# Performance work log

Measured on AMD Instinct MI355X. Metric: run time of the kernel, lower is better.

Reference implementation:

```python
import jax, jax.numpy as jnp
import numpy as np

B, P, ENC, DEC, ATT, EMB, V, MAXLEN = 64, 196, 2048, 1024, 1024, 1024, 10000, 20


def setup_inputs() -> dict:
    key = jax.random.key(0)
    ks = jax.random.split(key, 20)
    s = 0.02
    inp = {
        'encoder_out': jax.random.normal(ks[0], (B, 14, 14, ENC), jnp.float32),
        'encoded_captions': jax.random.randint(ks[1], (B, MAXLEN), 0, V),
        'caption_lengths': jax.random.randint(ks[2], (B, 1), 2, MAXLEN + 1).at[0, 0].set(MAXLEN),
        # embedding
        'emb_table': jax.random.uniform(ks[3], (V, EMB), jnp.float32, -0.1, 0.1),
        # attention MLP (weight_norm Linear == plain Linear math)
        'We': jax.random.normal(ks[4], (ATT, ENC)) * s,
        'be': jnp.zeros((ATT,), jnp.float32),
        'Wd': jax.random.normal(ks[5], (ATT, DEC)) * s,
        'bd': jnp.zeros((ATT,), jnp.float32),
        'Wf': jax.random.normal(ks[6], (1, ATT)) * s,
        'bf': jnp.zeros((1,), jnp.float32),
        # top_down_attention LSTMCell: input = EMB+ENC+DEC
        'W_ih1': jax.random.normal(ks[7], (4 * DEC, EMB + ENC + DEC)) * s,
        'W_hh1': jax.random.normal(ks[8], (4 * DEC, DEC)) * s,
        'b_ih1': jnp.zeros((4 * DEC,), jnp.float32),
        'b_hh1': jnp.zeros((4 * DEC,), jnp.float32),
        # language_model LSTMCell: input = ENC+DEC
        'W_ih2': jax.random.normal(ks[9], (4 * DEC, ENC + DEC)) * s,
        'W_hh2': jax.random.normal(ks[10], (4 * DEC, DEC)) * s,
        'b_ih2': jnp.zeros((4 * DEC,), jnp.float32),
        'b_hh2': jnp.zeros((4 * DEC,), jnp.float32),
        # output heads
        'Wfc1': jax.random.normal(ks[11], (V, DEC)) * s,
        'bfc1': jnp.zeros((V,), jnp.float32),
        'Wfc': jax.random.uniform(ks[12], (V, DEC), jnp.float32, -0.1, 0.1),
        'bfc': jnp.zeros((V,), jnp.float32),
    }
    return inp


def _lstm_cell(x, h, c, Wih, Whh, bih, bhh):
    g = x @ Wih.T + bih + h @ Whh.T + bhh
    i, f, gg, o = jnp.split(g, 4, axis=-1)  # torch gate order: i, f, g, o
    c2 = jax.nn.sigmoid(f) * c + jax.nn.sigmoid(i) * jnp.tanh(gg)
    h2 = jax.nn.sigmoid(o) * jnp.tanh(c2)
    return h2, c2


def _decode(encoder_out, encoded_captions, caption_lengths, emb_table,
            We, be, Wd, bd, Wf, bf,
            W_ih1, W_hh1, b_ih1, b_hh1, W_ih2, W_hh2, b_ih2, b_hh2,
            Wfc1, bfc1, Wfc, bfc):
    b = encoder_out.shape[0]
    enc = encoder_out.reshape(b, -1, encoder_out.shape[-1])  # (B,P,ENC)
    enc_mean = enc.mean(axis=1)
    cl = caption_lengths.squeeze(1)
    sort_ind = jnp.argsort(-cl)
    cl = cl[sort_ind]
    enc = enc[sort_ind]
    enc_mean = enc_mean[sort_ind]
    caps = encoded_captions[sort_ind]
    dec_len = cl - 1  # (B,)
    embeds = emb_table[caps]  # (B,T,EMB)
    Tdec = caps.shape[1] - 1
    # precompute encoder attention projection (loop-invariant, same math)
    att1 = jnp.einsum('bpe,ae->bpa', enc, We) + be  # (B,P,ATT)

    def step(carry, t):
        h1, c1, h2, c2 = carry
        active = (t < dec_len)[:, None]  # (B,1)
        x1 = jnp.concatenate([h2, enc_mean, embeds[:, t, :]], axis=1)
        h1n, c1n = _lstm_cell(x1, h1, c1, W_ih1, W_hh1, b_ih1, b_hh1)
        h1n = jnp.where(active, h1n, h1)
        c1n = jnp.where(active, c1n, c1)
        # Bahdanau attention
        att2 = h1n @ Wd.T + bd  # (B,ATT)
        e = jnp.einsum('bpa,a->bp', jax.nn.relu(att1 + att2[:, None, :]), Wf[0]) + bf[0]
        alpha = jax.nn.softmax(e, axis=1)
        awe = jnp.einsum('bpe,bp->be', enc, alpha)
        preds1 = h1n @ Wfc1.T + bfc1  # dropout is identity at eval
        x2 = jnp.concatenate([awe, h1n], axis=1)
        h2n, c2n = _lstm_cell(x2, h2, c2, W_ih2, W_hh2, b_ih2, b_hh2)
        h2n = jnp.where(active, h2n, h2)
        c2n = jnp.where(active, c2n, c2)
        preds = h2n @ Wfc.T + bfc
        preds = jnp.where(active, preds, 0.0)
        preds1 = jnp.where(active, preds1, 0.0)
        return (h1n, c1n, h2n, c2n), (preds, preds1)

    z = jnp.zeros((b, DEC), jnp.float32)
    (_, _, _, _), (pr, pr1) = jax.lax.scan(step, (z, z, z, z), jnp.arange(Tdec))
    predictions = jnp.transpose(pr, (1, 0, 2))  # (B,Tdec,V)
    predictions1 = jnp.transpose(pr1, (1, 0, 2))
    return predictions, predictions1, caps, dec_len, sort_ind


def reference(encoder_out, encoded_captions, caption_lengths, emb_table,
              We, be, Wd, bd, Wf, bf,
              W_ih1, W_hh1, b_ih1, b_hh1, W_ih2, W_hh2, b_ih2, b_hh2,
              Wfc1, bfc1, Wfc, bfc):
    return _decode(encoder_out, encoded_captions, caption_lengths, emb_table,
                   We, be, Wd, bd, Wf, bf,
                   W_ih1, W_hh1, b_ih1, b_hh1, W_ih2, W_hh2, b_ih2, b_hh2,
                   Wfc1, bfc1, Wfc, bfc)
```

## Files before the change

### kernel.cpp

```cpp
#include <hip/hip_runtime.h>
#include <cmath>

#define B_ 64
#define P_ 196
#define ENC_ 2048
#define DEC_ 1024
#define V_ 10000
#define MAXLEN_ 20
#define TDEC_ 19

typedef __attribute__((ext_vector_type(8))) short bf16x8;
typedef __attribute__((ext_vector_type(4))) float f32x4;


__device__ __align__(16) short g_encb[(size_t)12544 * 2048];
__device__ __align__(16) short g_encbt[(size_t)12544 * 2048];
__device__ __align__(16) short g_att1[(size_t)12544 * 1024];
__device__ __align__(16) short g_Wp1t[(size_t)4096 * 2048];
__device__ __align__(16) short g_Wemt[(size_t)4096 * 2048];
__device__ __align__(16) short g_Wembt[(size_t)4096 * 1024];
__device__ __align__(16) short g_Wc2t[(size_t)4096 * 4096];
__device__ __align__(16) short g_Webt[(size_t)1024 * 2048];
__device__ __align__(16) short g_Wdt[(size_t)1024 * 1024];
__device__ __align__(16) short g_Wfc1t[(size_t)10000 * 1024];
__device__ __align__(16) short g_Wfct[(size_t)10000 * 1024];
__device__ __align__(16) short g_xs1[(size_t)20 * 64 * 2048];
__device__ __align__(16) short g_xemb[(size_t)19 * 64 * 1024];
__device__ __align__(16) short g_xc2[(size_t)20 * 64 * 4096];
__device__ __align__(16) short g_em[64 * 2048];
__device__ __align__(16) float g_preemb[(size_t)19 * 64 * 4096];
__device__ __align__(16) float g_preem[64 * 4096];
__device__ __align__(16) float g_part[(size_t)16 * 64 * 4096];
__device__ __align__(16) float g_att2p[(size_t)8 * 64 * 1024];
__device__ __align__(16) float g_e[64 * P_];
__device__ __align__(16) float g_c1[64 * 1024];
__device__ __align__(16) float g_c2[64 * 1024];
__device__ int g_ibuf[64 + 64 + 64 * MAXLEN_];

__device__ __forceinline__ short f2b(float f) {
  unsigned u = __float_as_uint(f);
  u += 0x7FFFu + ((u >> 16) & 1u);
  return (short)(u >> 16);
}
__device__ __forceinline__ float b2f(short s) {
  return __uint_as_float(((unsigned)(unsigned short)s) << 16);
}

__global__ void k_sort(const int* __restrict__ cl_in, const int* __restrict__ caps_in,
                       int* __restrict__ sind, int* __restrict__ declen, int* __restrict__ caps_s,
                       float* __restrict__ out_caps, float* __restrict__ out_declen,
                       float* __restrict__ out_sind) {
  int i = threadIdx.x;
  __shared__ int cl[B_];
  cl[i] = cl_in[i];
  __syncthreads();
  int my = cl[i], pos = 0;
  for (int j = 0; j < B_; ++j) {
    int cj = cl[j];
    if (cj > my || (cj == my && j < i)) pos++;
  }
  sind[pos] = i;
  __syncthreads();
  int sb = sind[i];
  int dl = cl[sb] - 1;
  declen[i] = dl;
  out_declen[i] = (float)dl;
  out_sind[i] = (float)sb;
  for (int t = 0; t < MAXLEN_; ++t) {
    int v = caps_in[sb * MAXLEN_ + t];
    caps_s[i * MAXLEN_ + t] = v;
    out_caps[i * MAXLEN_ + t] = (float)v;
  }
}

__global__ __launch_bounds__(256) void k_encprep(const float* __restrict__ enc,
                                                 const int* __restrict__ sind,
                                                 short* __restrict__ encb,
                                                 short* __restrict__ encbt) {
  int mg = blockIdx.x;
  int b = mg / P_, p = mg - b * P_;
  int tid = threadIdx.x;
  const float* src = enc + ((size_t)sind[b] * P_ + p) * ENC_ + tid * 8;
  float4 a = *(const float4*)src;
  float4 c = *(const float4*)(src + 4);
  bf16x8 v;
  v[0] = f2b(a.x); v[1] = f2b(a.y); v[2] = f2b(a.z); v[3] = f2b(a.w);
  v[4] = f2b(c.x); v[5] = f2b(c.y); v[6] = f2b(c.z); v[7] = f2b(c.w);
  *(bf16x8*)(encb + (size_t)mg * ENC_ + tid * 8) = v;
  size_t off = (((size_t)(mg >> 4) * 64 + (tid >> 2)) << 9) +
               (((mg & 15) | ((tid & 3) << 4)) << 3);
  *(bf16x8*)(encbt + off) = v;
}

__global__ __launch_bounds__(64) void k_encmeanb(const short* __restrict__ encb,
                                                 short* __restrict__ em) {
  int b = blockIdx.x;
  int col0 = blockIdx.y * 512 + threadIdx.x * 8;
  const short* src = encb + (size_t)b * P_ * ENC_ + col0;
  float acc[8] = {};
  for (int p = 0; p < P_; ++p) {
    bf16x8 v = *(const bf16x8*)(src + (size_t)p * ENC_);
#pragma unroll
    for (int j = 0; j < 8; ++j) acc[j] += b2f(v[j]);
  }
#pragma unroll
  for (int j = 0; j < 8; ++j) em[b * 2048 + col0 + j] = f2b(acc[j] * (1.0f / 196.0f));
}

__global__ __launch_bounds__(256) void k_prefill(const float* __restrict__ emb,
                                                 const int* __restrict__ caps_s,
                                                 short* __restrict__ xemb) {
  int t = blockIdx.x, b = blockIdx.y, tid = threadIdx.x;
  short* xr = xemb + ((size_t)t * 64 + b) * 1024;
  int cap = caps_s[b * MAXLEN_ + t];
  int j = tid * 4;
  float4 v = *(const float4*)(emb + (size_t)cap * 1024 + j);
  short4 o;
  o.x = f2b(v.x); o.y = f2b(v.y); o.z = f2b(v.z); o.w = f2b(v.w);
  *(short4*)(xr + j) = o;
}

struct F2BJobs {
  const float* src[10];
  short* dst[10];
  int kstride[10];
  int c0[10];
  int ncols[10];
  int ktot[10];
  int koff[10];
  int base[11];
};

__global__ __launch_bounds__(256) void k_f2bt_all(F2BJobs jb) {
  int bg = blockIdx.x;
  int j = 0;
#pragma unroll
  for (int q = 1; q < 10; ++q)
    if (bg >= jb.base[q]) j = q;
  int wave = threadIdx.x >> 6, lane = threadIdx.x & 63;
  int tau = (bg - jb.base[j]) * 4 + wave;
  int ntk = jb.ncols[j] >> 5;
  int rt = tau / ntk, kt = tau - rt * ntk;
  int r = rt * 16 + (lane & 15);
  int k8 = kt * 32 + (lane >> 4) * 8;
  const float* s = jb.src[j] + (size_t)r * jb.kstride[j] + jb.c0[j] + k8;
  float4 a = *(const float4*)s;
  float4 c = *(const float4*)(s + 4);
  bf16x8 v;
  v[0] = f2b(a.x); v[1] = f2b(a.y); v[2] = f2b(a.z); v[3] = f2b(a.w);
  v[4] = f2b(c.x); v[5] = f2b(c.y); v[6] = f2b(c.z); v[7] = f2b(c.w);
  int kg0 = jb.koff[j] + kt * 32;
  size_t toff = (((size_t)rt * (jb.ktot[j] >> 5) + (kg0 >> 5)) << 9);
  *(bf16x8*)(jb.dst[j] + toff + lane * 8) = v;
}

__global__ __launch_bounds__(512) void k_att1_t(const short* __restrict__ At,
                                                const short* __restrict__ Wt,
                                                const float* __restrict__ be,
                                                short* __restrict__ Cb) {
  int wave = threadIdx.x >> 6, lane = threadIdx.x & 63;
  int mt0 = blockIdx.x * 8 + (wave >> 2) * 4;
  int nt0 = blockIdx.y * 16 + (wave & 3) * 4;
  f32x4 acc[4][4] = {};
  const short* Ab = At + ((size_t)mt0 * 64 << 9) + lane * 8;
  const short* Wb = Wt + ((size_t)nt0 * 64 << 9) + lane * 8;
  for (int kt = 0; kt < 64; ++kt) {
    bf16x8 a[4], b[4];
#pragma unroll
    for (int i = 0; i < 4; ++i) a[i] = *(const bf16x8*)(Ab + (((size_t)i * 64 + kt) << 9));
#pragma unroll
    for (int j = 0; j < 4; ++j) b[j] = *(const bf16x8*)(Wb + (((size_t)j * 64 + kt) << 9));
#pragma unroll
    for (int i = 0; i < 4; ++i)
#pragma unroll
      for (int j = 0; j < 4; ++j)
        acc[i][j] = __builtin_amdgcn_mfma_f32_16x16x32_bf16(a[i], b[j], acc[i][j], 0, 0, 0);
  }
  int rr = (lane >> 4) * 4, cc = lane & 15;
  int m0 = mt0 * 16, n0 = nt0 * 16;
#pragma unroll
  for (int i = 0; i < 4; ++i)
#pragma unroll
    for (int j = 0; j < 4; ++j) {
      int n = n0 + j * 16 + cc;
      float bn = be[n];
#pragma unroll
      for (int r = 0; r < 4; ++r) {
        int m = m0 + i * 16 + rr + r;
        Cb[(size_t)m * 1024 + n] = f2b(acc[i][j][r] + bn);
      }
    }
}

__global__ __launch_bounds__(256) void k_skinny_t(const short* __restrict__ A, int lda,
                                                  const short* __restrict__ Wt, int ldw,
                                                  int N, int kchunk, float* __restrict__ part) {
  int wave = threadIdx.x >> 6, lane = threadIdx.x & 63;
  int n0 = blockIdx.x * 128 + wave * 32;
  int kb = blockIdx.y * kchunk;
  int lr = lane & 15, lk = (lane >> 4) * 8;
  int ntk = ldw >> 5;
  int nt0 = n0 >> 4;
  f32x4 acc[4][2] = {};
  const short* Ab = A + (size_t)lr * lda + kb + lk;
  const short* Wb0 = Wt + (((size_t)nt0 * ntk + (kb >> 5)) << 9) + lane * 8;
  const short* Wb1 = Wt + (((size_t)(nt0 + 1) * ntk + (kb >> 5)) << 9) + lane * 8;
  int nkt = kchunk >> 5;
  for (int kt = 0; kt < nkt; ++kt) {
    bf16x8 a[4], b0, b1;
#pragma unroll
    for (int i = 0; i < 4; ++i) a[i] = *(const bf16x8*)(Ab + (size_t)i * 16 * lda + kt * 32);
    b0 = *(const bf16x8*)(Wb0 + ((size_t)kt << 9));
    b1 = *(const bf16x8*)(Wb1 + ((size_t)kt << 9));
#pragma unroll
    for (int i = 0; i < 4; ++i) {
      acc[i][0] = __builtin_amdgcn_mfma_f32_16x16x32_bf16(a[i], b0, acc[i][0], 0, 0, 0);
      acc[i][1] = __builtin_amdgcn_mfma_f32_16x16x32_bf16(a[i], b1, acc[i][1], 0, 0, 0);
    }
  }
  float* po = part + (size_t)blockIdx.y * 64 * N;
  int rr = (lane >> 4) * 4, cc = lane & 15;
#pragma unroll
  for (int i = 0; i < 4; ++i)
#pragma unroll
    for (int j = 0; j < 2; ++j) {
      int n = n0 + j * 16 + cc;
#pragma unroll
      for (int r = 0; r < 4; ++r) {
        int m = i * 16 + rr + r;
        po[(size_t)m * N + n] = acc[i][j][r];
      }
    }
}

__global__ void k_sumn(const float* __restrict__ part, int nsplit, float* __restrict__ dst) {
  int idx = blockIdx.x * 256 + threadIdx.x;
  float s = 0.0f;
  for (int q = 0; q < nsplit; ++q) s += part[(size_t)q * 64 * 4096 + idx];
  dst[idx] = s;
}

__global__ __launch_bounds__(256) void k_mid_emb4(const short* __restrict__ xemb,
                                                  const short* __restrict__ Wt,
                                                  float* __restrict__ preemb) {
  int wg = blockIdx.x;
  wg = (wg & 7) * 38 + (wg >> 3);
  int t = wg % 19;
  int nch = wg / 19;
  const short* A = xemb + (size_t)t * 64 * 1024;
  int wave = threadIdx.x >> 6, lane = threadIdx.x & 63;
  int nt0 = nch * 16 + wave * 4;
  int lr = lane & 15, lk = (lane >> 4) * 8;
  f32x4 acc[4][4] = {};
  const short* Ab = A + (size_t)lr * 1024 + lk;
  const short* Wb[4];
#pragma unroll
  for (int j = 0; j < 4; ++j) Wb[j] = Wt + ((size_t)(nt0 + j) * 32 << 9) + lane * 8;
  for (int kt = 0; kt < 32; ++kt) {
    bf16x8 a[4], b[4];
#pragma unroll
    for (int j = 0; j < 4; ++j) b[j] = *(const bf16x8*)(Wb[j] + ((size_t)kt << 9));
#pragma unroll
    for (int i = 0; i < 4; ++i) a[i] = *(const bf16x8*)(Ab + (size_t)i * 16 * 1024 + kt * 32);
#pragma unroll
    for (int i = 0; i < 4; ++i)
#pragma unroll
      for (int j = 0; j < 4; ++j)
        acc[i][j] = __builtin_amdgcn_mfma_f32_16x16x32_bf16(a[i], b[j], acc[i][j], 0, 0, 0);
  }
  float* po = preemb + (size_t)t * 64 * 4096;
  int rr = (lane >> 4) * 4, cc = lane & 15;
#pragma unroll
  for (int i = 0; i < 4; ++i)
#pragma unroll
    for (int j = 0; j < 4; ++j) {
      int n = (nt0 + j) * 16 + cc;
#pragma unroll
      for (int r = 0; r < 4; ++r) {
        int m = i * 16 + rr + r;
        po[(size_t)m * 4096 + n] = acc[i][j][r];
      }
    }
}

__global__ void k_gates(const float* __restrict__ part, int nsplit,
                        const float* __restrict__ pre, const float* __restrict__ pre2,
                        const float* __restrict__ bih, const float* __restrict__ bhh,
                        float* __restrict__ c,
                        const short* __restrict__ hold, int ldo,
                        short* __restrict__ dst1, int ld1,
                        short* __restrict__ dst2, int ld2,
                        const int* __restrict__ declen, int t) {
  int idx = blockIdx.x * 256 + threadIdx.x;
  int b = idx >> 10, j = idx & 1023;
  const float* pb = part + (size_t)b * 4096;
  float gi = bih[j] + bhh[j];
  float gf = bih[1024 + j] + bhh[1024 + j];
  float gg = bih[2048 + j] + bhh[2048 + j];
  float go = bih[3072 + j] + bhh[3072 + j];
  if (pre) {
    const float* pp = pre + (size_t)b * 4096;
    gi += pp[j]; gf += pp[j + 1024]; gg += pp[j + 2048]; go += pp[j + 3072];
  }
  if (pre2) {
    const float* pp = pre2 + (size_t)b * 4096;
    gi += pp[j]; gf += pp[j + 1024]; gg += pp[j + 2048]; go += pp[j + 3072];
  }
  for (int s = 0; s < nsplit; ++s) {
    const float* p = pb + (size_t)s * 64 * 4096;
    gi += p[j]; gf += p[j + 1024]; gg += p[j + 2048]; go += p[j + 3072];
  }
  float si = 1.0f / (1.0f + expf(-gi));
  float sf = 1.0f / (1.0f + expf(-gf));
  float so = 1.0f / (1.0f + expf(-go));
  float cn = sf * c[idx] + si * tanhf(gg);
  float hn = so * tanhf(cn);
  short hb;
  if (t < declen[b]) {
    c[idx] = cn;
    hb = f2b(hn);
  } else {
    hb = hold[b * ldo + j];
  }
  dst1[b * ld1 + j] = hb;
  dst2[b * ld2 + j] = hb;
}

__global__ __launch_bounds__(256) void k_e(const short* __restrict__ att1,
                                           const float* __restrict__ att2p,
                                           const float* __restrict__ bd,
                                           const float* __restrict__ Wf,
                                           const float* __restrict__ bf,
                                           float* __restrict__ e) {
  __shared__ float a2[1024];
  int b = blockIdx.x / 13, pq = blockIdx.x % 13;
  for (int i = threadIdx.x; i < 1024; i += 256) {
    float s = bd[i];
#pragma unroll
    for (int q = 0; q < 4; ++q) s += att2p[q * 65536 + b * 1024 + i];
    a2[i] = s;
  }
  __syncthreads();
  int wave = threadIdx.x >> 6, lane = threadIdx.x & 63;
#pragma unroll
  for (int i = 0; i < 4; ++i) {
    int p = pq * 16 + wave * 4 + i;
    if (p >= P_) break;
    const short* a1 = att1 + ((size_t)(b * P_ + p)) * 1024;
    float s = 0.0f;
#pragma unroll
    for (int h = 0; h < 2; ++h) {
      int k0 = lane * 8 + h * 512;
      bf16x8 v = *(const bf16x8*)(a1 + k0);
#pragma unroll
      for (int j = 0; j < 8; ++j) s += Wf[k0 + j] * fmaxf(b2f(v[j]) + a2[k0 + j], 0.0f);
    }
#pragma unroll
    for (int off = 32; off; off >>= 1) s += __shfl_down(s, off);
    if (lane == 0) e[b * P_ + p] = s + bf[0];
  }
}

__global__ __launch_bounds__(256) void k_sawe(const float* __restrict__ e,
                                              const short* __restrict__ encb,
                                              short* __restrict__ xc2t) {
  int b = blockIdx.x, ch = blockIdx.y;
  __shared__ float al[P_];
  __shared__ float red[8][256];
  int tid = threadIdx.x;
  if (tid < 64) {
    float vals[4];
    float mx = -1e30f;
#pragma unroll
    for (int q = 0; q < 4; ++q) {
      int p = tid + q * 64;
      vals[q] = (p < P_) ? e[b * P_ + p] : -1e30f;
      mx = fmaxf(mx, vals[q]);
    }
#pragma unroll
    for (int off = 32; off; off >>= 1) mx = fmaxf(mx, __shfl_xor(mx, off));
    float sum = 0.0f;
#pragma unroll
    for (int q = 0; q < 4; ++q) {
      int p = tid + q * 64;
      vals[q] = (p < P_) ? expf(vals[q] - mx) : 0.0f;
      sum += vals[q];
    }
#pragma unroll
    for (int off = 32; off; off >>= 1) sum += __shfl_xor(sum, off);
    float inv = 1.0f / sum;
#pragma unroll
    for (int q = 0; q < 4; ++q) {
      int p = tid + q * 64;
      if (p < P_) al[p] = vals[q] * inv;
    }
  }
  __syncthreads();
  int pg = tid >> 5, cg = tid & 31;
  int col = ch * 256 + cg * 8;
  const short* src = encb + (size_t)b * P_ * ENC_ + col;
  float acc[8] = {};
  for (int p = pg; p < P_; p += 8) {
    bf16x8 v = *(const bf16x8*)(src + (size_t)p * ENC_);
    float ap = al[p];
#pragma unroll
    for (int j = 0; j < 8; ++j) acc[j] += ap * b2f(v[j]);
  }
#pragma unroll
  for (int j = 0; j < 8; ++j) red[pg][cg * 8 + j] = acc[j];
  __syncthreads();
  float s = 0.0f;
#pragma unroll
  for (int g = 0; g < 8; ++g) s += red[g][tid];
  xc2t[b * 4096 + ch * 256 + tid] = f2b(s);
}

__global__ __launch_bounds__(256) void k_head4(const short* __restrict__ Aall,
                                               const short* __restrict__ Wt,
                                               const float* __restrict__ bias,
                                               float* __restrict__ outp,
                                               const int* __restrict__ declen) {
  int wg = blockIdx.x;
  wg = (wg & 7) * 95 + (wg >> 3);
  int t = wg % 19;
  int nch = wg / 19;
  const short* A = Aall + (size_t)t * (64 * 4096);
  int wave = threadIdx.x >> 6, lane = threadIdx.x & 63;
  int nt0 = nch * 16 + wave * 4;
  int lr = lane & 15, lk = (lane >> 4) * 8;
  f32x4 acc[4][4] = {};
  const short* Ab = A + (size_t)lr * 4096 + lk;
  const short* Wb[4];
  bool ok[4];
#pragma unroll
  for (int j = 0; j < 4; ++j) {
    ok[j] = (nt0 + j) < (V_ >> 4);
    Wb[j] = Wt + ((size_t)(ok[j] ? nt0 + j : 0) * 32 << 9) + lane * 8;
  }
  for (int kt = 0; kt < 32; ++kt) {
    bf16x8 a[4], b[4];
#pragma unroll
    for (int j = 0; j < 4; ++j) b[j] = *(const bf16x8*)(Wb[j] + ((size_t)kt << 9));
#pragma unroll
    for (int i = 0; i < 4; ++i) a[i] = *(const bf16x8*)(Ab + (size_t)i * 16 * 4096 + kt * 32);
#pragma unroll
    for (int i = 0; i < 4; ++i)
#pragma unroll
      for (int j = 0; j < 4; ++j)
        acc[i][j] = __builtin_amdgcn_mfma_f32_16x16x32_bf16(a[i], b[j], acc[i][j], 0, 0, 0);
  }
  int rr = (lane >> 4) * 4, cc = lane & 15;
#pragma unroll
  for (int j = 0; j < 4; ++j) {
    if (!ok[j]) continue;
    int n = (nt0 + j) * 16 + cc;
    float bn = bias[n];
#pragma unroll
    for (int i = 0; i < 4; ++i) {
#pragma unroll
      for (int r = 0; r < 4; ++r) {
        int b = i * 16 + rr + r;
        float val = acc[i][j][r] + bn;
        outp[((size_t)b * TDEC_ + t) * V_ + n] = (t < declen[b]) ? val : 0.0f;
      }
    }
  }
}

extern "C" void kernel_launch(void* const* d_in, const int* in_sizes, int n_in,
                              void* d_out, int out_size, void* d_ws, size_t ws_size,
                              hipStream_t stream) {
  (void)in_sizes; (void)n_in; (void)d_ws; (void)ws_size; (void)out_size;
  const float* enc  = (const float*)d_in[0];
  const int*   caps = (const int*)d_in[1];
  const int*   cl   = (const int*)d_in[2];
  const float* emb  = (const float*)d_in[3];
  const float* We   = (const float*)d_in[4];
  const float* be   = (const float*)d_in[5];
  const float* Wd   = (const float*)d_in[6];
  const float* bd   = (const float*)d_in[7];
  const float* Wf   = (const float*)d_in[8];
  const float* bf   = (const float*)d_in[9];
  const float* Wih1 = (const float*)d_in[10];
  const float* Whh1 = (const float*)d_in[11];
  const float* bih1 = (const float*)d_in[12];
  const float* bhh1 = (const float*)d_in[13];
  const float* Wih2 = (const float*)d_in[14];
  const float* Whh2 = (const float*)d_in[15];
  const float* bih2 = (const float*)d_in[16];
  const float* bhh2 = (const float*)d_in[17];
  const float* Wfc1 = (const float*)d_in[18];
  const float* bfc1 = (const float*)d_in[19];
  const float* Wfc  = (const float*)d_in[20];
  const float* bfc  = (const float*)d_in[21];
  float* out = (float*)d_out;

  short *encb, *encbt, *att1, *Wp1t, *Wemt, *Wembt, *Wc2t, *Webt, *Wdt, *Wfc1t, *Wfct;
  short *xs1, *xemb, *xc2, *em;
  float *preemb, *preem, *part, *att2p, *e, *c1, *c2;
  int* ib;
  hipGetSymbolAddress((void**)&encb, HIP_SYMBOL(g_encb));
  hipGetSymbolAddress((void**)&encbt, HIP_SYMBOL(g_encbt));
  hipGetSymbolAddress((void**)&att1, HIP_SYMBOL(g_att1));
  hipGetSymbolAddress((void**)&Wp1t, HIP_SYMBOL(g_Wp1t));
  hipGetSymbolAddress((void**)&Wemt, HIP_SYMBOL(g_Wemt));
  hipGetSymbolAddress((void**)&Wembt, HIP_SYMBOL(g_Wembt));
  hipGetSymbolAddress((void**)&Wc2t, HIP_SYMBOL(g_Wc2t));
  hipGetSymbolAddress((void**)&Webt, HIP_SYMBOL(g_Webt));
  hipGetSymbolAddress((void**)&Wdt, HIP_SYMBOL(g_Wdt));
  hipGetSymbolAddress((void**)&Wfc1t, HIP_SYMBOL(g_Wfc1t));
  hipGetSymbolAddress((void**)&Wfct, HIP_SYMBOL(g_Wfct));
  hipGetSymbolAddress((void**)&xs1, HIP_SYMBOL(g_xs1));
  hipGetSymbolAddress((void**)&xemb, HIP_SYMBOL(g_xemb));
  hipGetSymbolAddress((void**)&xc2, HIP_SYMBOL(g_xc2));
  hipGetSymbolAddress((void**)&em, HIP_SYMBOL(g_em));
  hipGetSymbolAddress((void**)&preemb, HIP_SYMBOL(g_preemb));
  hipGetSymbolAddress((void**)&preem, HIP_SYMBOL(g_preem));
  hipGetSymbolAddress((void**)&part, HIP_SYMBOL(g_part));
  hipGetSymbolAddress((void**)&att2p, HIP_SYMBOL(g_att2p));
  hipGetSymbolAddress((void**)&e, HIP_SYMBOL(g_e));
  hipGetSymbolAddress((void**)&c1, HIP_SYMBOL(g_c1));
  hipGetSymbolAddress((void**)&c2, HIP_SYMBOL(g_c2));
  hipGetSymbolAddress((void**)&ib, HIP_SYMBOL(g_ibuf));
  int* sind = ib;
  int* declen = ib + 64;
  int* caps_s = ib + 128;

  float* out_preds  = out;
  float* out_preds1 = out + (size_t)B_ * TDEC_ * V_;
  float* out_caps   = out + 2ull * B_ * TDEC_ * V_;
  float* out_declen = out_caps + B_ * MAXLEN_;
  float* out_sind   = out_declen + B_;

  k_sort<<<1, 64, 0, stream>>>(cl, caps, sind, declen, caps_s, out_caps, out_declen, out_sind);
  hipMemsetAsync(c1, 0, 64 * 1024 * sizeof(float), stream);
  hipMemsetAsync(c2, 0, 64 * 1024 * sizeof(float), stream);
  hipMemsetAsync(xs1, 0, (size_t)64 * 2048 * sizeof(short), stream);
  hipMemsetAsync(xc2, 0, (size_t)64 * 4096 * sizeof(short), stream);
  k_encprep<<<12544, 256, 0, stream>>>(enc, sind, encb, encbt);
  k_encmeanb<<<dim3(64, 4), 64, 0, stream>>>(encb, em);
  k_prefill<<<dim3(19, 64), 256, 0, stream>>>(emb, caps_s, xemb);
  {
    F2BJobs jb;
    const float* srcs[10] = {Wih1, Whh1, Wih1, Wih1, Wih2, Whh2, We, Wd, Wfc1, Wfc};
    short* dsts[10] = {Wp1t, Wp1t, Wemt, Wembt, Wc2t, Wc2t, Webt, Wdt, Wfc1t, Wfct};
    int kstride[10] = {4096, 1024, 4096, 4096, 3072, 1024, 2048, 1024, 1024, 1024};
    int c0s[10]     = {0, 0, 1024, 3072, 0, 0, 0, 0, 0, 0};
    int ncols[10]   = {1024, 1024, 2048, 1024, 3072, 1024, 2048, 1024, 1024, 1024};
    int ktots[10]   = {2048, 2048, 2048, 1024, 4096, 4096, 2048, 1024, 1024, 1024};
    int koffs[10]   = {0, 1024, 0, 0, 0, 3072, 0, 0, 0, 0};
    int nblk[10]    = {2048, 2048, 4096, 2048, 6144, 2048, 1024, 512, 5000, 5000};
    int cum = 0;
    for (int q = 0; q < 10; ++q) {
      jb.src[q] = srcs[q]; jb.dst[q] = dsts[q];
      jb.kstride[q] = kstride[q]; jb.c0[q] = c0s[q]; jb.ncols[q] = ncols[q];
      jb.ktot[q] = ktots[q]; jb.koff[q] = koffs[q];
      jb.base[q] = cum; cum += nblk[q];
    }
    jb.base[10] = cum;
    k_f2bt_all<<<cum, 256, 0, stream>>>(jb);
  }
  k_att1_t<<<dim3(98, 4), 512, 0, stream>>>(encbt, Webt, be, att1);
  k_skinny_t<<<dim3(32, 4), 256, 0, stream>>>(em, 2048, Wemt, 2048, 4096, 512, part);
  k_sumn<<<1024, 256, 0, stream>>>(part, 4, preem);
  k_mid_emb4<<<304, 256, 0, stream>>>(xemb, Wembt, preemb);

  for (int t = 0; t < TDEC_; ++t) {
    short* s1t = xs1 + (size_t)t * 64 * 2048;
    short* s1n = xs1 + (size_t)(t + 1) * 64 * 2048;
    short* x2t = xc2 + (size_t)t * 64 * 4096;
    short* x2n = xc2 + (size_t)(t + 1) * 64 * 4096;
    k_skinny_t<<<dim3(32, 8), 256, 0, stream>>>(s1t, 2048, Wp1t, 2048, 4096, 256, part);
    k_gates<<<256, 256, 0, stream>>>(part, 8, preemb + (size_t)t * 64 * 4096, preem,
                                     bih1, bhh1, c1, s1t + 1024, 2048,
                                     s1n + 1024, 2048, x2t + 2048, 4096, declen, t);
    k_skinny_t<<<dim3(8, 4), 256, 0, stream>>>(x2t + 2048, 4096, Wdt, 1024, 1024, 256, att2p);
    k_e<<<832, 256, 0, stream>>>(att1, att2p, bd, Wf, bf, e);
    k_sawe<<<dim3(64, 8), 256, 0, stream>>>(e, encb, x2t);
    k_skinny_t<<<dim3(32, 8), 256, 0, stream>>>(x2t, 4096, Wc2t, 4096, 4096, 512, part);
    k_gates<<<256, 256, 0, stream>>>(part, 8, nullptr, nullptr, bih2, bhh2, c2, s1t, 2048,
                                     s1n, 2048, x2n + 3072, 4096, declen, t);
  }
  k_head4<<<760, 256, 0, stream>>>(xc2 + 2048, Wfc1t, bfc1, out_preds1, declen);
  k_head4<<<760, 256, 0, stream>>>(xc2 + 64 * 4096 + 3072, Wfct, bfc, out_preds, declen);
}
```

Baseline: 1.696 ms.

## Fuse per-timestep decoder loop into one persistent cooperative kernel with grid syncs

Replaces the 19×7 separate kernel launches of the recurrent decode loop with a single cooperative kernel of 256 blocks that runs every phase (skinny GEMMs, gates, attention energy, softmax-weighted sum) and separates them with grid.sync(). This removes launch overhead and inter-kernel gaps on the serial critical path. In exchange, phases that used more blocks (k_e with 832, k_sawe with 512) now loop over work items inside fewer blocks. Small phases leave most blocks idle while they wait at the grid barrier.

```diff
diff --git a/kernel.cpp b/kernel.cpp
--- a/kernel.cpp
+++ b/kernel.cpp
@@ -1,5 +1,8 @@
 #include <hip/hip_runtime.h>
+#include <hip/hip_cooperative_groups.h>
 #include <cmath>
+
+namespace cg = cooperative_groups;
 
 #define B_ 64
 #define P_ 196
@@ -192,12 +195,12 @@
     }
 }
 
-__global__ __launch_bounds__(256) void k_skinny_t(const short* __restrict__ A, int lda,
-                                                  const short* __restrict__ Wt, int ldw,
-                                                  int N, int kchunk, float* __restrict__ part) {
-  int wave = threadIdx.x >> 6, lane = threadIdx.x & 63;
-  int n0 = blockIdx.x * 128 + wave * 32;
-  int kb = blockIdx.y * kchunk;
+__device__ __forceinline__ void skinny_phase(const short* __restrict__ A, int lda,
+                                             const short* __restrict__ Wt, int ldw,
+                                             int N, int kchunk, float* __restrict__ part,
+                                             int bx, int by, int wave, int lane) {
+  int n0 = bx * 128 + wave * 32;
+  int kb = by * kchunk;
   int lr = lane & 15, lk = (lane >> 4) * 8;
   int ntk = ldw >> 5;
   int nt0 = n0 >> 4;
@@ -218,7 +221,7 @@
       acc[i][1] = __builtin_amdgcn_mfma_f32_16x16x32_bf16(a[i], b1, acc[i][1], 0, 0, 0);
     }
   }
-  float* po = part + (size_t)blockIdx.y * 64 * N;
+  float* po = part + (size_t)by * 64 * N;
   int rr = (lane >> 4) * 4, cc = lane & 15;
 #pragma unroll
   for (int i = 0; i < 4; ++i)
@@ -231,6 +234,13 @@
         po[(size_t)m * N + n] = acc[i][j][r];
       }
     }
+}
+
+__global__ __launch_bounds__(256) void k_skinny_t(const short* __restrict__ A, int lda,
+                                                  const short* __restrict__ Wt, int ldw,
+                                                  int N, int kchunk, float* __restrict__ part) {
+  skinny_phase(A, lda, Wt, ldw, N, kchunk, part, blockIdx.x, blockIdx.y,
+               threadIdx.x >> 6, threadIdx.x & 63);
 }
 
 __global__ void k_sumn(const float* __restrict__ part, int nsplit, float* __restrict__ dst) {
@@ -283,15 +293,15 @@
     }
 }
 
-__global__ void k_gates(const float* __restrict__ part, int nsplit,
+__device__ __forceinline__ void gates_phase(const float* __restrict__ part, int nsplit,
                         const float* __restrict__ pre, const float* __restrict__ pre2,
                         const float* __restrict__ bih, const float* __restrict__ bhh,
                         float* __restrict__ c,
                         const short* __restrict__ hold, int ldo,
                         short* __restrict__ dst1, int ld1,
                         short* __restrict__ dst2, int ld2,
-                        const int* __restrict__ declen, int t) {
-  int idx = blockIdx.x * 256 + threadIdx.x;
+                        const int* __restrict__ declen, int t, int bid, int tid) {
+  int idx = bid * 256 + tid;
   int b = idx >> 10, j = idx & 1023;
   const float* pb = part + (size_t)b * 4096;
   float gi = bih[j] + bhh[j];
@@ -326,93 +336,123 @@
   dst2[b * ld2 + j] = hb;
 }
 
-__global__ __launch_bounds__(256) void k_e(const short* __restrict__ att1,
-                                           const float* __restrict__ att2p,
-                                           const float* __restrict__ bd,
-                                           const float* __restrict__ Wf,
-                                           const float* __restrict__ bf,
-                                           float* __restrict__ e) {
-  __shared__ float a2[1024];
-  int b = blockIdx.x / 13, pq = blockIdx.x % 13;
-  for (int i = threadIdx.x; i < 1024; i += 256) {
-    float s = bd[i];
-#pragma unroll
-    for (int q = 0; q < 4; ++q) s += att2p[q * 65536 + b * 1024 + i];
-    a2[i] = s;
-  }
-  __syncthreads();
-  int wave = threadIdx.x >> 6, lane = threadIdx.x & 63;
-#pragma unroll
-  for (int i = 0; i < 4; ++i) {
-    int p = pq * 16 + wave * 4 + i;
-    if (p >= P_) break;
-    const short* a1 = att1 + ((size_t)(b * P_ + p)) * 1024;
-    float s = 0.0f;
-#pragma unroll
-    for (int h = 0; h < 2; ++h) {
-      int k0 = lane * 8 + h * 512;
-      bf16x8 v = *(const bf16x8*)(a1 + k0);
-#pragma unroll
-      for (int j = 0; j < 8; ++j) s += Wf[k0 + j] * fmaxf(b2f(v[j]) + a2[k0 + j], 0.0f);
-    }
-#pragma unroll
-    for (int off = 32; off; off >>= 1) s += __shfl_down(s, off);
-    if (lane == 0) e[b * P_ + p] = s + bf[0];
-  }
-}
-
-__global__ __launch_bounds__(256) void k_sawe(const float* __restrict__ e,
-                                              const short* __restrict__ encb,
-                                              short* __restrict__ xc2t) {
-  int b = blockIdx.x, ch = blockIdx.y;
-  __shared__ float al[P_];
-  __shared__ float red[8][256];
-  int tid = threadIdx.x;
-  if (tid < 64) {
-    float vals[4];
-    float mx = -1e30f;
-#pragma unroll
-    for (int q = 0; q < 4; ++q) {
-      int p = tid + q * 64;
-      vals[q] = (p < P_) ? e[b * P_ + p] : -1e30f;
-      mx = fmaxf(mx, vals[q]);
-    }
-#pragma unroll
-    for (int off = 32; off; off >>= 1) mx = fmaxf(mx, __shfl_xor(mx, off));
-    float sum = 0.0f;
-#pragma unroll
-    for (int q = 0; q < 4; ++q) {
-      int p = tid + q * 64;
-      vals[q] = (p < P_) ? expf(vals[q] - mx) : 0.0f;
-      sum += vals[q];
-    }
-#pragma unroll
-    for (int off = 32; off; off >>= 1) sum += __shfl_xor(sum, off);
-    float inv = 1.0f / sum;
-#pragma unroll
-    for (int q = 0; q < 4; ++q) {
-      int p = tid + q * 64;
-      if (p < P_) al[p] = vals[q] * inv;
-    }
-  }
-  __syncthreads();
-  int pg = tid >> 5, cg = tid & 31;
-  int col = ch * 256 + cg * 8;
-  const short* src = encb + (size_t)b * P_ * ENC_ + col;
-  float acc[8] = {};
-  for (int p = pg; p < P_; p += 8) {
-    bf16x8 v = *(const bf16x8*)(src + (size_t)p * ENC_);
-    float ap = al[p];
-#pragma unroll
-    for (int j = 0; j < 8; ++j) acc[j] += ap * b2f(v[j]);
-  }
-#pragma unroll
-  for (int j = 0; j < 8; ++j) red[pg][cg * 8 + j] = acc[j];
-  __syncthreads();
-  float s = 0.0f;
-#pragma unroll
-  for (int g = 0; g < 8; ++g) s += red[g][tid];
-  xc2t[b * 4096 + ch * 256 + tid] = f2b(s);
+struct LoopArgs {
+  const short *Wp1t, *Wc2t, *Wdt, *att1, *encb;
+  const float *preemb, *preem, *bih1, *bhh1, *bih2, *bhh2, *bd, *Wf, *bf;
+  short *xs1, *xc2;
+  float *part, *att2p, *e, *c1, *c2;
+  const int* declen;
+};
+
+__global__ __launch_bounds__(256) void k_loop(LoopArgs La) {
+  cg::grid_group grid = cg::this_grid();
+  int bid = blockIdx.x, tid = threadIdx.x;
+  int wave = tid >> 6, lane = tid & 63;
+  __shared__ float smem[2304];
+
+  for (int t = 0; t < TDEC_; ++t) {
+    short* s1t = La.xs1 + (size_t)t * 64 * 2048;
+    short* s1n = La.xs1 + (size_t)(t + 1) * 64 * 2048;
+    short* x2t = La.xc2 + (size_t)t * 64 * 4096;
+    short* x2n = La.xc2 + (size_t)(t + 1) * 64 * 4096;
+
+    skinny_phase(s1t, 2048, La.Wp1t, 2048, 4096, 256, La.part, bid & 31, bid >> 5, wave, lane);
+    grid.sync();
+    gates_phase(La.part, 8, La.preemb + (size_t)t * 64 * 4096, La.preem,
+                La.bih1, La.bhh1, La.c1, s1t + 1024, 2048,
+                s1n + 1024, 2048, x2t + 2048, 4096, La.declen, t, bid, tid);
+    grid.sync();
+    if (bid < 32)
+      skinny_phase(x2t + 2048, 4096, La.Wdt, 1024, 1024, 256, La.att2p,
+                   bid & 7, bid >> 3, wave, lane);
+    grid.sync();
+    for (int w = bid; w < 832; w += 256) {
+      int b = w / 13, pq = w - b * 13;
+      __syncthreads();
+      for (int i = tid; i < 1024; i += 256) {
+        float s = La.bd[i];
+#pragma unroll
+        for (int q = 0; q < 4; ++q) s += La.att2p[q * 65536 + b * 1024 + i];
+        smem[i] = s;
+      }
+      __syncthreads();
+#pragma unroll
+      for (int i = 0; i < 4; ++i) {
+        int p = pq * 16 + wave * 4 + i;
+        if (p >= P_) break;
+        const short* a1 = La.att1 + ((size_t)(b * P_ + p)) * 1024;
+        float s = 0.0f;
+#pragma unroll
+        for (int h = 0; h < 2; ++h) {
+          int k0 = lane * 8 + h * 512;
+          bf16x8 v = *(const bf16x8*)(a1 + k0);
+#pragma unroll
+          for (int j = 0; j < 8; ++j) s += La.Wf[k0 + j] * fmaxf(b2f(v[j]) + smem[k0 + j], 0.0f);
+        }
+#pragma unroll
+        for (int off = 32; off; off >>= 1) s += __shfl_down(s, off);
+        if (lane == 0) La.e[b * P_ + p] = s + La.bf[0];
+      }
+    }
+    grid.sync();
+    for (int w = bid; w < 512; w += 256) {
+      int b = w >> 3, ch = w & 7;
+      float* al = smem;
+      float* red = smem + 256;
+      __syncthreads();
+      if (tid < 64) {
+        float vals[4];
+        float mx = -1e30f;
+#pragma unroll
+        for (int q = 0; q < 4; ++q) {
+          int p = tid + q * 64;
+          vals[q] = (p < P_) ? La.e[b * P_ + p] : -1e30f;
+          mx = fmaxf(mx, vals[q]);
+        }
+#pragma unroll
+        for (int off = 32; off; off >>= 1) mx = fmaxf(mx, __shfl_xor(mx, off));
+        float sum = 0.0f;
+#pragma unroll
+        for (int q = 0; q < 4; ++q) {
+          int p = tid + q * 64;
+          vals[q] = (p < P_) ? expf(vals[q] - mx) : 0.0f;
+          sum += vals[q];
+        }
+#pragma unroll
+        for (int off = 32; off; off >>= 1) sum += __shfl_xor(sum, off);
+        float inv = 1.0f / sum;
+#pragma unroll
+        for (int q = 0; q < 4; ++q) {
+          int p = tid + q * 64;
+          if (p < P_) al[p] = vals[q] * inv;
+        }
+      }
+      __syncthreads();
+      int pg = tid >> 5, cg = tid & 31;
+      int col = ch * 256 + cg * 8;
+      const short* src = La.encb + (size_t)b * P_ * ENC_ + col;
+      float acc[8] = {};
+      for (int p = pg; p < P_; p += 8) {
+        bf16x8 v = *(const bf16x8*)(src + (size_t)p * ENC_);
+        float ap = al[p];
+#pragma unroll
+        for (int j = 0; j < 8; ++j) acc[j] += ap * b2f(v[j]);
+      }
+#pragma unroll
+      for (int j = 0; j < 8; ++j) red[pg * 256 + cg * 8 + j] = acc[j];
+      __syncthreads();
+      float s = 0.0f;
+#pragma unroll
+      for (int g = 0; g < 8; ++g) s += red[g * 256 + tid];
+      x2t[b * 4096 + ch * 256 + tid] = f2b(s);
+    }
+    grid.sync();
+    skinny_phase(x2t, 4096, La.Wc2t, 4096, 4096, 512, La.part, bid & 31, bid >> 5, wave, lane);
+    grid.sync();
+    gates_phase(La.part, 8, nullptr, nullptr, La.bih2, La.bhh2, La.c2,
+                s1t, 2048, s1n, 2048, x2n + 3072, 4096, La.declen, t, bid, tid);
+    grid.sync();
+  }
 }
 
 __global__ __launch_bounds__(256) void k_head4(const short* __restrict__ Aall,
@@ -565,22 +605,19 @@
   k_sumn<<<1024, 256, 0, stream>>>(part, 4, preem);
   k_mid_emb4<<<304, 256, 0, stream>>>(xemb, Wembt, preemb);
 
-  for (int t = 0; t < TDEC_; ++t) {
-    short* s1t = xs1 + (size_t)t * 64 * 2048;
-    short* s1n = xs1 + (size_t)(t + 1) * 64 * 2048;
-    short* x2t = xc2 + (size_t)t * 64 * 4096;
-    short* x2n = xc2 + (size_t)(t + 1) * 64 * 4096;
-    k_skinny_t<<<dim3(32, 8), 256, 0, stream>>>(s1t, 2048, Wp1t, 2048, 4096, 256, part);
-    k_gates<<<256, 256, 0, stream>>>(part, 8, preemb + (size_t)t * 64 * 4096, preem,
-                                     bih1, bhh1, c1, s1t + 1024, 2048,
-                                     s1n + 1024, 2048, x2t + 2048, 4096, declen, t);
-    k_skinny_t<<<dim3(8, 4), 256, 0, stream>>>(x2t + 2048, 4096, Wdt, 1024, 1024, 256, att2p);
-    k_e<<<832, 256, 0, stream>>>(att1, att2p, bd, Wf, bf, e);
-    k_sawe<<<dim3(64, 8), 256, 0, stream>>>(e, encb, x2t);
-    k_skinny_t<<<dim3(32, 8), 256, 0, stream>>>(x2t, 4096, Wc2t, 4096, 4096, 512, part);
-    k_gates<<<256, 256, 0, stream>>>(part, 8, nullptr, nullptr, bih2, bhh2, c2, s1t, 2048,
-                                     s1n, 2048, x2n + 3072, 4096, declen, t);
-  }
+  {
+    LoopArgs la;
+    la.Wp1t = Wp1t; la.Wc2t = Wc2t; la.Wdt = Wdt; la.att1 = att1; la.encb = encb;
+    la.preemb = preemb; la.preem = preem;
+    la.bih1 = bih1; la.bhh1 = bhh1; la.bih2 = bih2; la.bhh2 = bhh2;
+    la.bd = bd; la.Wf = Wf; la.bf = bf;
+    la.xs1 = xs1; la.xc2 = xc2;
+    la.part = part; la.att2p = att2p; la.e = e; la.c1 = c1; la.c2 = c2;
+    la.declen = declen;
+    void* params[] = {&la};
+    hipLaunchCooperativeKernel((const void*)k_loop, dim3(256), dim3(256), params, 0, stream);
+  }
+
   k_head4<<<760, 256, 0, stream>>>(xc2 + 2048, Wfc1t, bfc1, out_preds1, declen);
   k_head4<<<760, 256, 0, stream>>>(xc2 + 64 * 4096 + 3072, Wfct, bfc, out_preds, declen);
 }
```

After: 6.018 ms. 255% more time.
